# Performance work log

Hardware: AMD Instinct MI355X
Metric: run time of the kernel (lower is better)

## Reference

```python
import jax, jax.numpy as jnp
import numpy as np

NUM_HEADS = 16


def setup_inputs() -> dict:
    key = jax.random.key(0)
    ks = jax.random.split(key, 8)
    B, S, E = 2, 2048, 1024
    std = 0.02
    return {
        "q": jax.random.normal(ks[0], (B, S, E), dtype=jnp.float32),
        "k": jax.random.normal(ks[1], (B, S, E), dtype=jnp.float32),
        "v": jax.random.normal(ks[2], (B, S, E), dtype=jnp.float32),
        "Wq": jax.random.normal(ks[3], (E, E), dtype=jnp.float32) * std,
        "Wk": jax.random.normal(ks[4], (E, E), dtype=jnp.float32) * std,
        "Wv": jax.random.normal(ks[5], (E, E), dtype=jnp.float32) * std,
        "Wo": jax.random.normal(ks[6], (E, E), dtype=jnp.float32) * std,
        "bo": jnp.zeros((E,), dtype=jnp.float32),
    }


def reference(q, k, v, Wq, Wk, Wv, Wo, bo):
    B, S, E = q.shape
    H = NUM_HEADS
    D = E // H
    # projections (nn.Linear: x @ W.T)
    Q = (q @ Wq.T).reshape(B, S, H, D).transpose(0, 2, 1, 3)  # [B,H,S,D]
    K = (k @ Wk.T).reshape(B, S, H, D).transpose(0, 2, 1, 3)
    V = (v @ Wv.T).reshape(B, S, H, D).transpose(0, 2, 1, 3)
    scores = jnp.einsum("bhsd,bhtd->bhst", Q, K)  # [B,H,S,S]
    # causal mask applied before scaling (as in source; -inf/sqrt(d) == -inf)
    causal = jnp.tril(jnp.ones((S, S), dtype=bool))
    scores = jnp.where(causal, scores, -jnp.inf)
    scores = scores / np.sqrt(D).astype(np.float32)
    attn = jax.nn.softmax(scores, axis=-1)
    out = jnp.einsum("bhst,bhtd->bhsd", attn, V)  # [B,H,S,D]
    out = out.transpose(0, 2, 1, 3).reshape(B, S, E)
    return out @ Wo.T + bo
```

## Files before the change

kernel.cpp:

```cpp
#include <hip/hip_runtime.h>

typedef unsigned short u16;
typedef __bf16 bf16x8 __attribute__((ext_vector_type(8)));
typedef float f32x4 __attribute__((ext_vector_type(4)));
typedef unsigned u32x4 __attribute__((ext_vector_type(4)));

#define B_ 2
#define S_ 2048
#define E_ 1024
#define H_ 16
#define D_ 64
#define M_ (B_ * S_)

__device__ inline u16 f2bf(float f) {
  union { float f; unsigned int u; } c; c.f = f;
  unsigned int u = c.u;
  return (u16)((u + 0x7FFFu + ((u >> 16) & 1u)) >> 16);
}

__device__ inline f32x4 mfma16(bf16x8 a, bf16x8 b, f32x4 c) {
  return __builtin_amdgcn_mfma_f32_16x16x32_bf16(a, b, c, 0, 0, 0);
}

__device__ inline void gload16(const void* g, void* lds) {
  __builtin_amdgcn_global_load_lds(
      (const __attribute__((address_space(1))) unsigned int*)g,
      (__attribute__((address_space(3))) unsigned int*)lds, 16, 0, 0);
}

struct CvtArgs {
  const float* src[7];
  u16* dst[7];
  int n[7];
};

__global__ __launch_bounds__(256) void cvt_kernel(CvtArgs a) {
  const int arr = blockIdx.y;
  const int n = a.n[arr];
  const float* __restrict__ s = a.src[arr];
  u16* __restrict__ d = a.dst[arr];
  const int stride = gridDim.x * blockDim.x;
  for (int i = blockIdx.x * blockDim.x + threadIdx.x; i * 4 < n; i += stride) {
    const float4 f = *(const float4*)(s + 4 * i);
    ushort4 o;
    o.x = f2bf(f.x); o.y = f2bf(f.y); o.z = f2bf(f.z); o.w = f2bf(f.w);
    *(ushort4*)(d + 4 * i) = o;
  }
}

__global__ __launch_bounds__(256, 3) void qkv_gemm(
    const u16* __restrict__ qb, const u16* __restrict__ kb,
    const u16* __restrict__ vbp, const u16* __restrict__ Wqb,
    const u16* __restrict__ Wkb, const u16* __restrict__ Wvb,
    u16* __restrict__ Qh, u16* __restrict__ Kh, u16* __restrict__ Vt) {
  constexpr int BM = 128, BN = 128, BK = 32;
  __shared__ alignas(16) u16 As[3][BM * BK];
  __shared__ alignas(16) u16 Bs[3][BN * BK];

  const int wg = blockIdx.x;
  const int xcd = wg & 7, idx = wg >> 3;
  const int nb = idx & 7, mz = idx >> 3;
  const int z = mz >> 2;
  const int m0 = (xcd * 4 + (mz & 3)) * BM, n0 = nb * BN;

  const u16* A  = (z == 0) ? qb  : (z == 1) ? kb  : vbp;
  const u16* Bt = (z == 0) ? Wqb : (z == 1) ? Wkb : Wvb;
  u16* outp     = (z == 0) ? Qh  : (z == 1) ? Kh  : Vt;

  const int tid = threadIdx.x;
  const int wave = tid >> 6, lane = tid & 63;
  const int wm = (wave >> 1) * 64, wn = (wave & 1) * 64;
  const int fr = lane & 15, fc = lane >> 4;
  const int lrow = lane >> 2;
  const int lcol_sw = (((lane & 3) ^ ((lrow >> 1) & 3)) * 8);

  f32x4 acc[4][4] = {};

  u16 *aA = As[0], *aB = As[1], *aC = As[2];
  u16 *bA = Bs[0], *bB = Bs[1], *bC = Bs[2];

  auto stage = [&](int k0, u16* as, u16* bs) {
#pragma unroll
    for (int i = 0; i < 2; ++i) {
      const int chunk = wave * 2 + i;
      const int row = chunk * 16 + lrow;
      gload16(A + (size_t)(m0 + row) * E_ + k0 + lcol_sw, as + chunk * 16 * BK);
      gload16(Bt + (size_t)(n0 + row) * E_ + k0 + lcol_sw, bs + chunk * 16 * BK);
    }
  };

  constexpr int NK = E_ / BK;
  stage(0, aA, bA);
  stage(BK, aB, bB);

  const int sl = (fc ^ ((fr >> 1) & 3)) * 8;

  for (int t = 0; t < NK; ++t) {
    if (t + 1 < NK) {
      asm volatile("s_waitcnt vmcnt(4)" ::: "memory");
    } else {
      asm volatile("s_waitcnt vmcnt(0)" ::: "memory");
    }
    __builtin_amdgcn_s_barrier();
    __builtin_amdgcn_sched_barrier(0);

    if (t + 2 < NK) stage((t + 2) * BK, aC, bC);

    bf16x8 af[4], bfr[4];
#pragma unroll
    for (int mi = 0; mi < 4; ++mi)
      af[mi] = *(const bf16x8*)&aA[(wm + mi * 16 + fr) * BK + sl];
#pragma unroll
    for (int ni = 0; ni < 4; ++ni)
      bfr[ni] = *(const bf16x8*)&bA[(wn + ni * 16 + fr) * BK + sl];
    __builtin_amdgcn_s_setprio(1);
#pragma unroll
    for (int mi = 0; mi < 4; ++mi)
#pragma unroll
      for (int ni = 0; ni < 4; ++ni)
        acc[mi][ni] = mfma16(af[mi], bfr[ni], acc[mi][ni]);
    __builtin_amdgcn_s_setprio(0);

    u16* tp;
    tp = aA; aA = aB; aB = aC; aC = tp;
    tp = bA; bA = bB; bB = bC; bC = tp;
  }

#pragma unroll
  for (int mi = 0; mi < 4; ++mi)
#pragma unroll
    for (int ni = 0; ni < 4; ++ni)
#pragma unroll
      for (int r = 0; r < 4; ++r) {
        const int m = m0 + wm + mi * 16 + (fc << 2) + r;
        const int n = n0 + wn + ni * 16 + fr;
        const float v = acc[mi][ni][r];
        const int b = m >> 11, s = m & (S_ - 1), h = n >> 6, d = n & 63;
        if (z != 2) {
          outp[((((size_t)b * H_ + h) * S_ + s) << 6) + d] = f2bf(v);
        } else {
          outp[(((size_t)b * H_ + h) * D_ + d) * S_ + s] = f2bf(v);
        }
      }
}

__global__ __launch_bounds__(256, 4) void oproj_gemm(
    const u16* __restrict__ A, const u16* __restrict__ Bt,
    const float* __restrict__ bias, float* __restrict__ outp) {
  constexpr int BM = 64, BN = 128, BK = 32;
  constexpr int ACH = BM / 16, NCH = ACH + BN / 16;
  __shared__ alignas(16) u16 As[BM * BK];
  __shared__ alignas(16) u16 Bs[BN * BK];
  const int tid = threadIdx.x;
  const int wave = tid >> 6, lane = tid & 63;
  const int m0 = blockIdx.y * BM, n0 = blockIdx.x * BN;
  const int wm = (wave >> 1) * 32, wn = (wave & 1) * 64;
  const int lrow = lane >> 2, lcol = (lane & 3) * 8;

  f32x4 acc[2][4] = {};

  for (int k0 = 0; k0 < E_; k0 += BK) {
#pragma unroll
    for (int c = wave; c < NCH; c += 4) {
      if (c < ACH)
        gload16(A + (size_t)(m0 + c * 16 + lrow) * E_ + k0 + lcol, As + c * 16 * BK);
      else
        gload16(Bt + (size_t)(n0 + (c - ACH) * 16 + lrow) * E_ + k0 + lcol,
                Bs + (c - ACH) * 16 * BK);
    }
    __syncthreads();
    bf16x8 af[2], bfr[4];
#pragma unroll
    for (int mi = 0; mi < 2; ++mi)
      af[mi] = *(const bf16x8*)&As[(wm + mi * 16 + (lane & 15)) * BK + 8 * (lane >> 4)];
#pragma unroll
    for (int ni = 0; ni < 4; ++ni)
      bfr[ni] = *(const bf16x8*)&Bs[(wn + ni * 16 + (lane & 15)) * BK + 8 * (lane >> 4)];
#pragma unroll
    for (int mi = 0; mi < 2; ++mi)
#pragma unroll
      for (int ni = 0; ni < 4; ++ni)
        acc[mi][ni] = mfma16(af[mi], bfr[ni], acc[mi][ni]);
    __syncthreads();
  }

#pragma unroll
  for (int mi = 0; mi < 2; ++mi)
#pragma unroll
    for (int ni = 0; ni < 4; ++ni)
#pragma unroll
      for (int r = 0; r < 4; ++r) {
        const int m = m0 + wm + mi * 16 + ((lane >> 4) << 2) + r;
        const int n = n0 + wn + ni * 16 + (lane & 15);
        outp[(size_t)m * E_ + n] = acc[mi][ni][r] + bias[n];
      }
}

__device__ __forceinline__ void stage_kv(
    const u16* __restrict__ Kh_head, const u16* __restrict__ Vt_head,
    int kv0, u16* kb, u16* vb, int wq, int lane) {
#pragma unroll
  for (int i = 0; i < 2; ++i) {
    const int c = 2 * wq + i;
    gload16(Kh_head + (size_t)(kv0 + lane) * D_ + c * 8, kb + c * 512);
    gload16(Vt_head + (size_t)lane * S_ + kv0 + c * 8, vb + c * 512);
  }
}

__global__ __launch_bounds__(256, 2) void flash_attn(
    const u16* __restrict__ Qh, const u16* __restrict__ Kh,
    const u16* __restrict__ Vt, u16* __restrict__ O) {
  __shared__ alignas(16) u16 Kb[3][4096];
  __shared__ alignas(16) u16 Vb[3][4096];

  const int j = blockIdx.x;
  const int qt = 31 - (j >> 5);
  const int bh = j & 31;

  const int tid = threadIdx.x;
  const int wq = tid >> 6, lane = tid & 63;

  const int q0 = qt * 64;
  const int b = bh >> 4, h = bh & 15;
  constexpr float SC = 0.125f * 1.4426950408889634f;
  const int fr = lane & 15, fc = lane >> 4;

  const u16* Qbase = Qh + ((size_t)bh * S_ + q0 + wq * 16 + fr) * D_ + 8 * fc;
  const bf16x8 qf0 = *(const bf16x8*)Qbase;
  const bf16x8 qf1 = *(const bf16x8*)(Qbase + 32);
  const u16* Kh_head = Kh + (size_t)bh * S_ * D_;
  const u16* Vt_head = Vt + (size_t)bh * D_ * S_;

  float lacc = 0.f;
  f32x4 oacc[4] = {};
  const int nt = qt + 1;

  u16 *kA = Kb[0], *kB = Kb[1], *kC = Kb[2];
  u16 *vA = Vb[0], *vB = Vb[1], *vC = Vb[2];

  stage_kv(Kh_head, Vt_head, 0, kA, vA, wq, lane);
  stage_kv(Kh_head, Vt_head, 64, kB, vB, wq, lane);

  for (int t = 0; t < nt; ++t) {
    if (t + 1 < nt) {
      asm volatile("s_waitcnt vmcnt(4)" ::: "memory");
    } else {
      asm volatile("s_waitcnt vmcnt(0)" ::: "memory");
    }
    __builtin_amdgcn_s_barrier();
    __builtin_amdgcn_sched_barrier(0);

    if (t + 2 < nt)
      stage_kv(Kh_head, Vt_head, (t + 2) * 64, kC, vC, wq, lane);

    const u16* kb = kA;
    const u16* vb = vA;

    f32x4 sacc[4] = {};
    __builtin_amdgcn_s_setprio(1);
#pragma unroll
    for (int ni = 0; ni < 4; ++ni) {
      const bf16x8 k0 = *(const bf16x8*)&kb[fc * 512 + (16 * ni + fr) * 8];
      const bf16x8 k1 = *(const bf16x8*)&kb[(fc + 4) * 512 + (16 * ni + fr) * 8];
      sacc[ni] = mfma16(k0, qf0, sacc[ni]);
      sacc[ni] = mfma16(k1, qf1, sacc[ni]);
    }
    __builtin_amdgcn_s_setprio(0);

    const bool diag = (t == qt);
    const int qloc = wq * 16 + fr;
#pragma unroll
    for (int ni = 0; ni < 4; ++ni)
#pragma unroll
      for (int r = 0; r < 4; ++r) {
        const int kvloc = 16 * ni + 4 * fc + r;
        float pv;
        if (diag && kvloc > qloc) {
          pv = 0.f;
        } else {
          pv = __builtin_amdgcn_exp2f(sacc[ni][r] * SC);
        }
        sacc[ni][r] = pv;
        lacc += pv;
      }

    unsigned w[4][2];
#pragma unroll
    for (int ni = 0; ni < 4; ++ni) {
      asm("v_cvt_pk_bf16_f32 %0, %1, %2"
          : "=v"(w[ni][0]) : "v"(sacc[ni][0]), "v"(sacc[ni][1]));
      asm("v_cvt_pk_bf16_f32 %0, %1, %2"
          : "=v"(w[ni][1]) : "v"(sacc[ni][2]), "v"(sacc[ni][3]));
    }

    unsigned paw0[4], paw1[4];
#pragma unroll
    for (int pair = 0; pair < 2; ++pair) {
      unsigned xx[2], yy[2], tt[2];
#pragma unroll
      for (int hh = 0; hh < 2; ++hh) {
        unsigned a = w[2 * pair][hh], bb = w[2 * pair + 1][hh];
        asm volatile("v_permlane32_swap_b32 %0, %1" : "+v"(a), "+v"(bb));
        xx[hh] = a; yy[hh] = bb;
        const unsigned s = (fc & 1) ? a : bb;
        tt[hh] = (unsigned)__shfl_xor((int)s, 16);
      }
      unsigned* pw_ = pair ? paw1 : paw0;
      pw_[0] = (fc & 1) ? tt[0] : xx[0];
      pw_[1] = (fc & 1) ? tt[1] : xx[1];
      pw_[2] = (fc & 1) ? yy[0] : tt[0];
      pw_[3] = (fc & 1) ? yy[1] : tt[1];
    }
    bf16x8 pa0, pa1;
    {
      u32x4 t0 = {paw0[0], paw0[1], paw0[2], paw0[3]};
      u32x4 t1 = {paw1[0], paw1[1], paw1[2], paw1[3]};
      __builtin_memcpy(&pa0, &t0, 16);
      __builtin_memcpy(&pa1, &t1, 16);
    }

    __builtin_amdgcn_s_setprio(1);
#pragma unroll
    for (int nd = 0; nd < 4; ++nd) {
      const bf16x8 v0 = *(const bf16x8*)&vb[fc * 512 + (16 * nd + fr) * 8];
      const bf16x8 v1 = *(const bf16x8*)&vb[(fc + 4) * 512 + (16 * nd + fr) * 8];
      oacc[nd] = mfma16(pa0, v0, oacc[nd]);
      oacc[nd] = mfma16(pa1, v1, oacc[nd]);
    }
    __builtin_amdgcn_s_setprio(0);

    u16* tk = kA; kA = kB; kB = kC; kC = tk;
    u16* tv = vA; vA = vB; vB = vC; vC = tv;
  }

  float l = lacc;
  l += __shfl_xor(l, 16);
  l += __shfl_xor(l, 32);
  float linv[4];
#pragma unroll
  for (int r = 0; r < 4; ++r)
    linv[r] = __builtin_amdgcn_rcpf(__shfl(l, 4 * fc + r));

#pragma unroll
  for (int nd = 0; nd < 4; ++nd) {
#pragma unroll
    for (int r = 0; r < 4; ++r) {
      const int qr = q0 + wq * 16 + (fc << 2) + r;
      const int d = 16 * nd + fr;
      const float v = oacc[nd][r] * linv[r];
      O[((size_t)b * S_ + qr) * E_ + h * D_ + d] = f2bf(v);
    }
  }
}

extern "C" void kernel_launch(void* const* d_in, const int* in_sizes, int n_in,
                              void* d_out, int out_size, void* d_ws, size_t ws_size,
                              hipStream_t stream) {
  const float* q  = (const float*)d_in[0];
  const float* k  = (const float*)d_in[1];
  const float* v  = (const float*)d_in[2];
  const float* Wq = (const float*)d_in[3];
  const float* Wk = (const float*)d_in[4];
  const float* Wv = (const float*)d_in[5];
  const float* Wo = (const float*)d_in[6];
  const float* bo = (const float*)d_in[7];

  const size_t nBSE = (size_t)M_ * E_;
  const size_t nEE  = (size_t)E_ * E_;
  u16* qb  = (u16*)d_ws;
  u16* kb  = qb + nBSE;
  u16* vb  = kb + nBSE;
  u16* Wqb = vb + nBSE;
  u16* Wkb = Wqb + nEE;
  u16* Wvb = Wkb + nEE;
  u16* Wob = Wvb + nEE;
  u16* Qh  = Wob + nEE;
  u16* Kh  = Qh + nBSE;
  u16* Vt  = qb;
  u16* Oa  = vb;

  CvtArgs ca;
  ca.src[0] = q;  ca.dst[0] = qb;  ca.n[0] = (int)nBSE;
  ca.src[1] = k;  ca.dst[1] = kb;  ca.n[1] = (int)nBSE;
  ca.src[2] = v;  ca.dst[2] = vb;  ca.n[2] = (int)nBSE;
  ca.src[3] = Wq; ca.dst[3] = Wqb; ca.n[3] = (int)nEE;
  ca.src[4] = Wk; ca.dst[4] = Wkb; ca.n[4] = (int)nEE;
  ca.src[5] = Wv; ca.dst[5] = Wvb; ca.n[5] = (int)nEE;
  ca.src[6] = Wo; ca.dst[6] = Wob; ca.n[6] = (int)nEE;
  cvt_kernel<<<dim3(512, 7), 256, 0, stream>>>(ca);

  qkv_gemm<<<dim3(768), 256, 0, stream>>>(
      qb, kb, vb, Wqb, Wkb, Wvb, Qh, Kh, Vt);
  flash_attn<<<dim3(1024), 256, 0, stream>>>(Qh, Kh, Vt, Oa);
  oproj_gemm<<<dim3(E_ / 128, M_ / 64), 256, 0, stream>>>(Oa, Wob, bo, (float*)d_out);
}
```

Before: 122.2 us.

## Triple-buffer output projection GEMM and widen flash-attention blocks to 128 query rows

The output-projection GEMM moves from a single-buffered loop with two __syncthreads per step to a three-stage async prefetch pipeline. It also adds XOR-swizzled LDS layout, MFMA priority hints and an XCD-aware block mapping. Flash attention now uses 512-thread blocks covering 128 query rows, so each staged K/V tile is shared by 8 waves, and a serpentine block ordering balances causal work. This aims to hide global-load latency and raise K/V reuse, at the cost of larger blocks and fewer blocks in the grid.

```diff
diff --git a/kernel.cpp b/kernel.cpp
--- a/kernel.cpp
+++ b/kernel.cpp
@@ -148,40 +148,73 @@
     const u16* __restrict__ A, const u16* __restrict__ Bt,
     const float* __restrict__ bias, float* __restrict__ outp) {
   constexpr int BM = 64, BN = 128, BK = 32;
-  constexpr int ACH = BM / 16, NCH = ACH + BN / 16;
-  __shared__ alignas(16) u16 As[BM * BK];
-  __shared__ alignas(16) u16 Bs[BN * BK];
+  __shared__ alignas(16) u16 As[3][BM * BK];
+  __shared__ alignas(16) u16 Bs[3][BN * BK];
+
+  const int wg = blockIdx.x;
+  const int xcd = wg & 7, idx = wg >> 3;
+  const int nb = idx & 7, mi_ = idx >> 3;
+  const int m0 = (xcd * 8 + mi_) * BM, n0 = nb * BN;
+
   const int tid = threadIdx.x;
   const int wave = tid >> 6, lane = tid & 63;
-  const int m0 = blockIdx.y * BM, n0 = blockIdx.x * BN;
   const int wm = (wave >> 1) * 32, wn = (wave & 1) * 64;
-  const int lrow = lane >> 2, lcol = (lane & 3) * 8;
+  const int fr = lane & 15, fc = lane >> 4;
+  const int lrow = lane >> 2;
+  const int lcol_sw = (((lane & 3) ^ ((lrow >> 1) & 3)) * 8);
 
   f32x4 acc[2][4] = {};
 
-  for (int k0 = 0; k0 < E_; k0 += BK) {
-#pragma unroll
-    for (int c = wave; c < NCH; c += 4) {
-      if (c < ACH)
-        gload16(A + (size_t)(m0 + c * 16 + lrow) * E_ + k0 + lcol, As + c * 16 * BK);
+  u16 *aA = As[0], *aB = As[1], *aC = As[2];
+  u16 *bA = Bs[0], *bB = Bs[1], *bC = Bs[2];
+
+  auto stage = [&](int k0, u16* as, u16* bs) {
+#pragma unroll
+    for (int i = 0; i < 3; ++i) {
+      const int c = wave + 4 * i;
+      if (c < 4)
+        gload16(A + (size_t)(m0 + c * 16 + lrow) * E_ + k0 + lcol_sw, as + c * 16 * BK);
       else
-        gload16(Bt + (size_t)(n0 + (c - ACH) * 16 + lrow) * E_ + k0 + lcol,
-                Bs + (c - ACH) * 16 * BK);
-    }
-    __syncthreads();
+        gload16(Bt + (size_t)(n0 + (c - 4) * 16 + lrow) * E_ + k0 + lcol_sw,
+                bs + (c - 4) * 16 * BK);
+    }
+  };
+
+  constexpr int NK = E_ / BK;
+  stage(0, aA, bA);
+  stage(BK, aB, bB);
+
+  const int sl = (fc ^ ((fr >> 1) & 3)) * 8;
+
+  for (int t = 0; t < NK; ++t) {
+    if (t + 1 < NK) {
+      asm volatile("s_waitcnt vmcnt(3)" ::: "memory");
+    } else {
+      asm volatile("s_waitcnt vmcnt(0)" ::: "memory");
+    }
+    __builtin_amdgcn_s_barrier();
+    __builtin_amdgcn_sched_barrier(0);
+
+    if (t + 2 < NK) stage((t + 2) * BK, aC, bC);
+
     bf16x8 af[2], bfr[4];
 #pragma unroll
     for (int mi = 0; mi < 2; ++mi)
-      af[mi] = *(const bf16x8*)&As[(wm + mi * 16 + (lane & 15)) * BK + 8 * (lane >> 4)];
+      af[mi] = *(const bf16x8*)&aA[(wm + mi * 16 + fr) * BK + sl];
 #pragma unroll
     for (int ni = 0; ni < 4; ++ni)
-      bfr[ni] = *(const bf16x8*)&Bs[(wn + ni * 16 + (lane & 15)) * BK + 8 * (lane >> 4)];
+      bfr[ni] = *(const bf16x8*)&bA[(wn + ni * 16 + fr) * BK + sl];
+    __builtin_amdgcn_s_setprio(1);
 #pragma unroll
     for (int mi = 0; mi < 2; ++mi)
 #pragma unroll
       for (int ni = 0; ni < 4; ++ni)
         acc[mi][ni] = mfma16(af[mi], bfr[ni], acc[mi][ni]);
-    __syncthreads();
+    __builtin_amdgcn_s_setprio(0);
+
+    u16* tp;
+    tp = aA; aA = aB; aB = aC; aC = tp;
+    tp = bA; bA = bB; bB = bC; bC = tp;
   }
 
 #pragma unroll
@@ -190,37 +223,36 @@
     for (int ni = 0; ni < 4; ++ni)
 #pragma unroll
       for (int r = 0; r < 4; ++r) {
-        const int m = m0 + wm + mi * 16 + ((lane >> 4) << 2) + r;
-        const int n = n0 + wn + ni * 16 + (lane & 15);
+        const int m = m0 + wm + mi * 16 + (fc << 2) + r;
+        const int n = n0 + wn + ni * 16 + fr;
         outp[(size_t)m * E_ + n] = acc[mi][ni][r] + bias[n];
       }
 }
 
-__device__ __forceinline__ void stage_kv(
+
+__device__ __forceinline__ void stage_kv8(
     const u16* __restrict__ Kh_head, const u16* __restrict__ Vt_head,
     int kv0, u16* kb, u16* vb, int wq, int lane) {
-#pragma unroll
-  for (int i = 0; i < 2; ++i) {
-    const int c = 2 * wq + i;
-    gload16(Kh_head + (size_t)(kv0 + lane) * D_ + c * 8, kb + c * 512);
-    gload16(Vt_head + (size_t)lane * S_ + kv0 + c * 8, vb + c * 512);
-  }
-}
-
-__global__ __launch_bounds__(256, 2) void flash_attn(
+  gload16(Kh_head + (size_t)(kv0 + lane) * D_ + wq * 8, kb + wq * 512);
+  gload16(Vt_head + (size_t)lane * S_ + kv0 + wq * 8, vb + wq * 512);
+}
+
+__global__ __launch_bounds__(512, 4) void flash_attn(
     const u16* __restrict__ Qh, const u16* __restrict__ Kh,
     const u16* __restrict__ Vt, u16* __restrict__ O) {
   __shared__ alignas(16) u16 Kb[3][4096];
   __shared__ alignas(16) u16 Vb[3][4096];
 
-  const int j = blockIdx.x;
-  const int qt = 31 - (j >> 5);
+  const int i = blockIdx.x;
+  const int ch = i >> 8, p = i & 255;
+  const int j = (ch << 8) + ((ch & 1) ? (255 - p) : p);
+  const int qt = 15 - (j >> 5);
   const int bh = j & 31;
 
   const int tid = threadIdx.x;
   const int wq = tid >> 6, lane = tid & 63;
 
-  const int q0 = qt * 64;
+  const int q0 = qt * 128;
   const int b = bh >> 4, h = bh & 15;
   constexpr float SC = 0.125f * 1.4426950408889634f;
   const int fr = lane & 15, fc = lane >> 4;
@@ -233,17 +265,17 @@
 
   float lacc = 0.f;
   f32x4 oacc[4] = {};
-  const int nt = qt + 1;
+  const int nt = 2 * qt + 2;
 
   u16 *kA = Kb[0], *kB = Kb[1], *kC = Kb[2];
   u16 *vA = Vb[0], *vB = Vb[1], *vC = Vb[2];
 
-  stage_kv(Kh_head, Vt_head, 0, kA, vA, wq, lane);
-  stage_kv(Kh_head, Vt_head, 64, kB, vB, wq, lane);
+  stage_kv8(Kh_head, Vt_head, 0, kA, vA, wq, lane);
+  stage_kv8(Kh_head, Vt_head, 64, kB, vB, wq, lane);
 
   for (int t = 0; t < nt; ++t) {
     if (t + 1 < nt) {
-      asm volatile("s_waitcnt vmcnt(4)" ::: "memory");
+      asm volatile("s_waitcnt vmcnt(2)" ::: "memory");
     } else {
       asm volatile("s_waitcnt vmcnt(0)" ::: "memory");
     }
@@ -251,7 +283,7 @@
     __builtin_amdgcn_sched_barrier(0);
 
     if (t + 2 < nt)
-      stage_kv(Kh_head, Vt_head, (t + 2) * 64, kC, vC, wq, lane);
+      stage_kv8(Kh_head, Vt_head, (t + 2) * 64, kC, vC, wq, lane);
 
     const u16* kb = kA;
     const u16* vb = vA;
@@ -267,15 +299,16 @@
     }
     __builtin_amdgcn_s_setprio(0);
 
-    const bool diag = (t == qt);
-    const int qloc = wq * 16 + fr;
+    const bool diag = (t >= nt - 2);
+    const int qg = q0 + wq * 16 + fr;
+    const int kvb = t * 64;
 #pragma unroll
     for (int ni = 0; ni < 4; ++ni)
 #pragma unroll
       for (int r = 0; r < 4; ++r) {
-        const int kvloc = 16 * ni + 4 * fc + r;
+        const int kvg = kvb + 16 * ni + 4 * fc + r;
         float pv;
-        if (diag && kvloc > qloc) {
+        if (diag && kvg > qg) {
           pv = 0.f;
         } else {
           pv = __builtin_amdgcn_exp2f(sacc[ni][r] * SC);
@@ -391,6 +424,6 @@
 
   qkv_gemm<<<dim3(768), 256, 0, stream>>>(
       qb, kb, vb, Wqb, Wkb, Wvb, Qh, Kh, Vt);
-  flash_attn<<<dim3(1024), 256, 0, stream>>>(Qh, Kh, Vt, Oa);
-  oproj_gemm<<<dim3(E_ / 128, M_ / 64), 256, 0, stream>>>(Oa, Wob, bo, (float*)d_out);
-}
+  flash_attn<<<dim3(512), 512, 0, stream>>>(Qh, Kh, Vt, Oa);
+  oproj_gemm<<<dim3(512), 256, 0, stream>>>(Oa, Wob, bo, (float*)d_out);
+}
```

Measured after the change: 115.5 us. 1.06x faster.
